# Kernel tuning notes

Measured on AMD Instinct MI355X. Metric: run time of the kernel, lower is better.

Reference implementation:

```python
import jax, jax.numpy as jnp
import numpy as np

N, K, CIN, HID, COUT, E, MH = 8192, 200, 512, 256, 40, 5, 64
KG = K // E
EPS = 1e-5


def setup_inputs() -> dict:
    key = jax.random.key(0)
    ks = jax.random.split(key, 20)
    inp = {
        "X": jax.random.normal(ks[0], (N, CIN), jnp.float32),
        "La": jax.random.uniform(ks[1], (K,), jnp.float32),
        "U": jax.random.normal(ks[2], (N, K), jnp.float32),
        # 5 EigenExperts, each mlp = Linear(1,64) -> ReLU -> Linear(64,64) -> ReLU -> Linear(64,1)
        "eW1": jax.random.normal(ks[3], (E, MH), jnp.float32) * 0.5,
        "eb1": jax.random.normal(ks[4], (E, MH), jnp.float32) * 0.1,
        "eW2": jax.random.normal(ks[5], (E, MH, MH), jnp.float32) * (1.0 / np.sqrt(MH)),
        "eb2": jax.random.normal(ks[6], (E, MH), jnp.float32) * 0.1,
        "eW3": jax.random.normal(ks[7], (E, MH), jnp.float32) * (1.0 / np.sqrt(MH)),
        "eb3": jax.random.normal(ks[8], (E,), jnp.float32) * 0.1,
        # gate: Linear(5,5) -> ReLU -> Linear(5,5) -> Softmax
        "gW1": jax.random.normal(ks[9], (E, E), jnp.float32) * 0.4,
        "gb1": jax.random.normal(ks[10], (E,), jnp.float32) * 0.1,
        "gW2": jax.random.normal(ks[11], (E, E), jnp.float32) * 0.4,
        "gb2": jax.random.normal(ks[12], (E,), jnp.float32) * 0.1,
        # W: Linear(in_channels, hidden_dim)
        "Ww": jax.random.normal(ks[13], (CIN, HID), jnp.float32) * (1.0 / np.sqrt(CIN)),
        "Wb": jax.random.normal(ks[14], (HID,), jnp.float32) * 0.1,
        # BatchNorm1d(hidden_dim), training-mode batch stats
        "bn_gamma": jnp.ones((HID,), jnp.float32),
        "bn_beta": jnp.zeros((HID,), jnp.float32),
        # MLP: Linear(hidden_dim, out_channels)
        "Mw": jax.random.normal(ks[15], (HID, COUT), jnp.float32) * (1.0 / np.sqrt(HID)),
        "Mb": jax.random.normal(ks[16], (COUT,), jnp.float32) * 0.1,
    }
    return inp


def reference(X, La, U, eW1, eb1, eW2, eb2, eW3, eb3, gW1, gb1, gW2, gb2, Ww, Wb, bn_gamma, bn_beta, Mw, Mb):
    n, k = U.shape
    e = eW1.shape[0]
    kg = k // e
    # group eigenvector columns: U[:, i*kg:(i+1)*kg] for expert i -> [n, e, kg]
    Ue = U.reshape(n, e, kg)
    # EigenExpert tiny MLP applied elementwise over entries of each column, then mean over nodes
    h1 = jax.nn.relu(jnp.einsum('nek,eh->nekh', Ue, eW1) + eb1[None, :, None, :])
    h2 = jax.nn.relu(jnp.einsum('nekh,ehg->nekg', h1, eW2) + eb2[None, :, None, :])
    v = jnp.einsum('nekh,eh->nek', h2, eW3) + eb3[None, :, None]
    V = v.mean(axis=0)                      # [e, kg] importance per eigenvector
    # gate on per-group mean eigenvalue
    stats = La.reshape(e, kg).mean(axis=1)  # [e]
    g = jax.nn.relu(stats @ gW1 + gb1) @ gW2 + gb2
    g = jax.nn.softmax(g, axis=-1)          # [e]
    # sum_i g_i * U_i diag(V_i) U_i^T == (U * s) @ U^T with per-column scale s
    s = (g[:, None] * V).reshape(k)         # [k]
    A = (U * s[None, :]) @ U.T              # [n, n]
    out = A @ X                             # [n, cin]
    hidden = out @ Ww + Wb                  # [n, hid]
    mu = hidden.mean(axis=0)
    var = hidden.var(axis=0)                # biased, as torch BN uses for normalization
    h = (hidden - mu) * jax.lax.rsqrt(var + EPS) * bn_gamma + bn_beta
    h = jax.nn.relu(h)                      # dropout is identity (eval)
    logits = h @ Mw + Mb
    return jax.nn.log_softmax(logits, axis=1), hidden
```

## Files before the change

### kernel.cpp

```cpp
#include <hip/hip_runtime.h>
#include <hip/hip_bf16.h>

#define N_    8192
#define K_    200
#define CIN_  512
#define HID_  256
#define COUT_ 40
#define E_    5
#define MH_   64
#define KG_   40
#define EPS_  1e-5f

#define WS_VSUM  0
#define WS_BNSUM 256
#define WS_T     768
#define WS_S     103168
#define WS_G     103424

typedef __bf16 bf16x8 __attribute__((ext_vector_type(8)));
typedef _Float16 f16x2 __attribute__((ext_vector_type(2)));
typedef _Float16 f16x8 __attribute__((ext_vector_type(8)));
typedef float  f32x16 __attribute__((ext_vector_type(16)));

__device__ __forceinline__ uint packbf(float a, float b) {
    union { __bf16 h[2]; uint u; } p;
    p.h[0] = (__bf16)a; p.h[1] = (__bf16)b;
    return p.u;
}

union UB { uint4 q; bf16x8 v; };
union UHF { f16x2 h2[4]; f16x8 v; };

__global__ __launch_bounds__(256) void k_expert(
    const float* __restrict__ U,
    const float* __restrict__ eW1, const float* __restrict__ eb1,
    const float* __restrict__ eW2, const float* __restrict__ eb2,
    const float* __restrict__ eW3, const float* __restrict__ eb3,
    float* __restrict__ Vsum)
{
    const int e   = blockIdx.x;
    const int tid = threadIdx.x;
    const int w   = tid >> 6;
    const int l   = tid & 63;
    const int lo  = l & 31;
    const int hi  = l >> 5;

    __shared__ f16x2 sW1h[32], sb1h[32];
    __shared__ float sb2s[MH_], sW3s[MH_];
    __shared__ float colsum[KG_];

    if (tid < 32) {
        f16x2 w2; w2.x = (_Float16)eW1[e*MH_ + 2*tid]; w2.y = (_Float16)eW1[e*MH_ + 2*tid + 1];
        sW1h[tid] = w2;
        f16x2 b2; b2.x = (_Float16)eb1[e*MH_ + 2*tid]; b2.y = (_Float16)eb1[e*MH_ + 2*tid + 1];
        sb1h[tid] = b2;
    }
    if (tid < MH_) {
        sb2s[tid] = eb2[e*MH_ + tid];
        sW3s[tid] = eW3[e*MH_ + tid];
    }
    if (tid < KG_) colsum[tid] = 0.f;
    const float b3 = eb3[e];

    UHF fa[2][4];
    {
        const float* W2e = eW2 + e*MH_*MH_;
        #pragma unroll
        for (int mt = 0; mt < 2; ++mt) {
            const int grow = mt*32 + lo;
            #pragma unroll
            for (int t = 0; t < 4; ++t) {
                const int k0 = 16*t + 8*hi;
                #pragma unroll
                for (int r = 0; r < 4; ++r) {
                    f16x2 p;
                    p.x = (_Float16)W2e[(k0+2*r  )*MH_ + grow];
                    p.y = (_Float16)W2e[(k0+2*r+1)*MH_ + grow];
                    fa[mt][t].h2[r] = p;
                }
            }
        }
    }
    __syncthreads();

    float uu[4]; int kgs[4];
    {
        const int idx0 = (blockIdx.y*16 + w)*64 + l;
        int n = idx0 / KG_, kg = idx0 - n*KG_;
        #pragma unroll
        for (int it = 0; it < 4; ++it) {
            uu[it]  = U[n*K_ + e*KG_ + kg];
            kgs[it] = kg;
            kg += 16; if (kg >= KG_) { kg -= KG_; n += 1; }
            n += 6;
        }
    }

    const f16x2 z2 = {(_Float16)0.f, (_Float16)0.f};

    #pragma unroll
    for (int it = 0; it < 4; ++it) {
        const float ucol0 = __shfl(uu[it], lo);
        const float ucol1 = __shfl(uu[it], 32 + lo);
        f16x2 u20; u20.x = (_Float16)ucol0; u20.y = (_Float16)ucol0;
        f16x2 u21; u21.x = (_Float16)ucol1; u21.y = (_Float16)ucol1;

        f32x16 acc00 = {0}; f32x16 acc10 = {0};
        f32x16 acc01 = {0}; f32x16 acc11 = {0};
        #pragma unroll
        for (int t = 0; t < 4; ++t) {
            const int kp = 8*t + 4*hi;
            UHF b0, b1;
            #pragma unroll
            for (int r = 0; r < 4; ++r) {
                const f16x2 w1  = sW1h[kp + r];
                const f16x2 b1c = sb1h[kp + r];
                b0.h2[r] = __builtin_elementwise_max(u20*w1 + b1c, z2);
                b1.h2[r] = __builtin_elementwise_max(u21*w1 + b1c, z2);
            }
            acc00 = __builtin_amdgcn_mfma_f32_32x32x16_f16(fa[0][t].v, b0.v, acc00, 0, 0, 0);
            acc10 = __builtin_amdgcn_mfma_f32_32x32x16_f16(fa[1][t].v, b0.v, acc10, 0, 0, 0);
            acc01 = __builtin_amdgcn_mfma_f32_32x32x16_f16(fa[0][t].v, b1.v, acc01, 0, 0, 0);
            acc11 = __builtin_amdgcn_mfma_f32_32x32x16_f16(fa[1][t].v, b1.v, acc11, 0, 0, 0);
        }

        float vs0 = 0.f, vs1 = 0.f;
        #pragma unroll
        for (int r = 0; r < 16; ++r) {
            const int gb  = (r & 3) + 8*(r >> 2) + 4*hi;
            const float b2a = sb2s[gb],      w3a = sW3s[gb];
            const float b2b = sb2s[32 + gb], w3b = sW3s[32 + gb];
            vs0 += fmaxf(acc00[r] + b2a, 0.f)*w3a + fmaxf(acc10[r] + b2b, 0.f)*w3b;
            vs1 += fmaxf(acc01[r] + b2a, 0.f)*w3a + fmaxf(acc11[r] + b2b, 0.f)*w3b;
        }
        vs0 += __shfl_xor(vs0, 32);
        vs1 += __shfl_xor(vs1, 32);

        const float myv = (hi ? vs1 : vs0) + b3;
        atomicAdd(&colsum[kgs[it]], myv);
    }

    __syncthreads();
    if (tid < KG_) atomicAdd(&Vsum[e*KG_ + tid], colsum[tid]);
}

__global__ void k_gate(
    const float* __restrict__ La,
    const float* __restrict__ gW1, const float* __restrict__ gb1,
    const float* __restrict__ gW2, const float* __restrict__ gb2,
    const float* __restrict__ Vsum, float* __restrict__ s)
{
    __shared__ float sg[E_];
    const int tid = threadIdx.x;
    if (tid == 0) {
        float stats[E_], g1[E_], g2[E_];
        for (int e = 0; e < E_; ++e) {
            float acc = 0.f;
            for (int k = 0; k < KG_; ++k) acc += La[e*KG_ + k];
            stats[e] = acc * (1.0f/KG_);
        }
        for (int j = 0; j < E_; ++j) {
            float acc = gb1[j];
            for (int i = 0; i < E_; ++i) acc += stats[i]*gW1[i*E_ + j];
            g1[j] = fmaxf(acc, 0.f);
        }
        float m = -1e30f;
        for (int j = 0; j < E_; ++j) {
            float acc = gb2[j];
            for (int i = 0; i < E_; ++i) acc += g1[i]*gW2[i*E_ + j];
            g2[j] = acc;
            m = fmaxf(m, acc);
        }
        float ssum = 0.f;
        for (int j = 0; j < E_; ++j) { g2[j] = expf(g2[j]-m); ssum += g2[j]; }
        for (int j = 0; j < E_; ++j) sg[j] = g2[j] / ssum;
    }
    __syncthreads();
    if (tid < K_) s[tid] = sg[tid / KG_] * Vsum[tid] * (1.0f/N_);
}

__global__ __launch_bounds__(256) void k_utx(
    const float* __restrict__ U, const float* __restrict__ X,
    float* __restrict__ P)
{
    const int nc0 = blockIdx.x * 64;
    const int mc0 = blockIdx.y * 64;
    const int ks  = blockIdx.z;
    const int r0  = ks * 512;
    const int tid = threadIdx.x;
    const int w   = tid >> 6, l = tid & 63, lo = l & 31, hi = l >> 5;
    const int mq  = w >> 1, nq = w & 1;

    __shared__ uint sU[2][32][68];
    __shared__ uint sX[2][32][68];

    const int rpA = tid >> 4;
    const int rpB = rpA + 16;
    const int c4  = tid & 15;
    const int mcA = mc0 + 4*c4;
    const int xcA = nc0 + 4*c4;
    const int UMAX = N_*K_ - 4;

    float4 uA0,uA1,uB0,uB1,xA0,xA1,xB0,xB1;

#define UTX_LD(chunk) {                                                       \
    const int rb_ = r0 + 64*(chunk);                                          \
    uA0 = *reinterpret_cast<const float4*>(&U[min((rb_+2*rpA  )*K_ + mcA, UMAX)]); \
    uA1 = *reinterpret_cast<const float4*>(&U[min((rb_+2*rpA+1)*K_ + mcA, UMAX)]); \
    uB0 = *reinterpret_cast<const float4*>(&U[min((rb_+2*rpB  )*K_ + mcA, UMAX)]); \
    uB1 = *reinterpret_cast<const float4*>(&U[min((rb_+2*rpB+1)*K_ + mcA, UMAX)]); \
    xA0 = *reinterpret_cast<const float4*>(&X[(rb_+2*rpA  )*CIN_ + xcA]);     \
    xA1 = *reinterpret_cast<const float4*>(&X[(rb_+2*rpA+1)*CIN_ + xcA]);     \
    xB0 = *reinterpret_cast<const float4*>(&X[(rb_+2*rpB  )*CIN_ + xcA]);     \
    xB1 = *reinterpret_cast<const float4*>(&X[(rb_+2*rpB+1)*CIN_ + xcA]); }

#define UTX_WR(buf) {                                                         \
    uint4 p_;                                                                 \
    p_.x = packbf(uA0.x,uA1.x); p_.y = packbf(uA0.y,uA1.y);                   \
    p_.z = packbf(uA0.z,uA1.z); p_.w = packbf(uA0.w,uA1.w);                   \
    *reinterpret_cast<uint4*>(&sU[buf][rpA][4*c4]) = p_;                      \
    p_.x = packbf(uB0.x,uB1.x); p_.y = packbf(uB0.y,uB1.y);                   \
    p_.z = packbf(uB0.z,uB1.z); p_.w = packbf(uB0.w,uB1.w);                   \
    *reinterpret_cast<uint4*>(&sU[buf][rpB][4*c4]) = p_;                      \
    p_.x = packbf(xA0.x,xA1.x); p_.y = packbf(xA0.y,xA1.y);                   \
    p_.z = packbf(xA0.z,xA1.z); p_.w = packbf(xA0.w,xA1.w);                   \
    *reinterpret_cast<uint4*>(&sX[buf][rpA][4*c4]) = p_;                      \
    p_.x = packbf(xB0.x,xB1.x); p_.y = packbf(xB0.y,xB1.y);                   \
    p_.z = packbf(xB0.z,xB1.z); p_.w = packbf(xB0.w,xB1.w);                   \
    *reinterpret_cast<uint4*>(&sX[buf][rpB][4*c4]) = p_; }

#define UTX_MM(buf) {                                                         \
    _Pragma("unroll") for (int ksi = 0; ksi < 4; ++ksi) {                     \
        const int rp0_ = 8*ksi + 4*hi;                                        \
        UB a_, b_;                                                            \
        a_.q.x = sU[buf][rp0_+0][32*mq+lo];                                   \
        a_.q.y = sU[buf][rp0_+1][32*mq+lo];                                   \
        a_.q.z = sU[buf][rp0_+2][32*mq+lo];                                   \
        a_.q.w = sU[buf][rp0_+3][32*mq+lo];                                   \
        b_.q.x = sX[buf][rp0_+0][32*nq+lo];                                   \
        b_.q.y = sX[buf][rp0_+1][32*nq+lo];                                   \
        b_.q.z = sX[buf][rp0_+2][32*nq+lo];                                   \
        b_.q.w = sX[buf][rp0_+3][32*nq+lo];                                   \
        acc = __builtin_amdgcn_mfma_f32_32x32x16_bf16(a_.v, b_.v, acc, 0,0,0); } }

    f32x16 acc = {0};
    UTX_LD(0);
    UTX_WR(0);
    __syncthreads();
    #pragma unroll
    for (int t = 0; t < 8; ++t) {
        if (t < 7) UTX_LD(t+1);
        UTX_MM(t & 1);
        if (t < 7) UTX_WR((t+1) & 1);
        __syncthreads();
    }

    #pragma unroll
    for (int r = 0; r < 16; ++r) {
        const int mrow = mc0 + mq*32 + (r & 3) + 8*(r >> 2) + 4*hi;
        const int ncol = nc0 + nq*32 + lo;
        P[(ks*256 + mrow)*512 + ncol] = acc[r];
    }
#undef UTX_LD
#undef UTX_WR
#undef UTX_MM
}

__global__ __launch_bounds__(256) void k_red(
    const float* __restrict__ P, float* __restrict__ T)
{
    const int j  = blockIdx.x*256 + threadIdx.x;
    const int m  = j >> 7;
    const int c4 = j & 127;
    float4 s4 = {0.f, 0.f, 0.f, 0.f};
    for (int ks = 0; ks < 16; ++ks) {
        const float4 v = *reinterpret_cast<const float4*>(&P[(ks*256 + m)*512 + 4*c4]);
        s4.x += v.x; s4.y += v.y; s4.z += v.z; s4.w += v.w;
    }
    *reinterpret_cast<float4*>(&T[m*512 + 4*c4]) = s4;
}

__global__ __launch_bounds__(256) void k_g(
    const float* __restrict__ T, const float* __restrict__ Ww,
    float* __restrict__ G)
{
    const int k0  = blockIdx.x * 4;
    const int c   = threadIdx.x;
    __shared__ float4 sT4[4][128];

    for (int j = threadIdx.x; j < 512; j += 256) {
        const int r = j >> 7, c4 = j & 127;
        sT4[r][c4] = reinterpret_cast<const float4*>(T)[(k0+r)*128 + c4];
    }
    __syncthreads();

    float a0 = 0.f, a1 = 0.f, a2 = 0.f, a3 = 0.f;
    for (int ci4 = 0; ci4 < 128; ++ci4) {
        const float w0 = Ww[(4*ci4+0)*HID_ + c];
        const float w1 = Ww[(4*ci4+1)*HID_ + c];
        const float w2 = Ww[(4*ci4+2)*HID_ + c];
        const float w3 = Ww[(4*ci4+3)*HID_ + c];
        float4 t;
        t = sT4[0][ci4]; a0 += t.x*w0 + t.y*w1 + t.z*w2 + t.w*w3;
        t = sT4[1][ci4]; a1 += t.x*w0 + t.y*w1 + t.z*w2 + t.w*w3;
        t = sT4[2][ci4]; a2 += t.x*w0 + t.y*w1 + t.z*w2 + t.w*w3;
        t = sT4[3][ci4]; a3 += t.x*w0 + t.y*w1 + t.z*w2 + t.w*w3;
    }
    G[(k0+0)*HID_ + c] = a0;
    G[(k0+1)*HID_ + c] = a1;
    G[(k0+2)*HID_ + c] = a2;
    G[(k0+3)*HID_ + c] = a3;
}

__global__ __launch_bounds__(256) void k_hidden(
    const float* __restrict__ U, const float* __restrict__ s,
    const float* __restrict__ G, const float* __restrict__ Wb,
    float* __restrict__ hid, float* __restrict__ bnsum)
{
    const int c0  = blockIdx.x * 32;
    const int n0  = blockIdx.y * 128;
    const int tid = threadIdx.x;
    const int w   = tid >> 6;
    const int l   = tid & 63;
    const int lo  = l & 31;
    const int hi  = l >> 5;

    __shared__ uint  sA[104][129];
    __shared__ uint  sB[104][33];
    __shared__ float ss[208];

    if (tid < 208) ss[tid] = (tid < K_) ? s[tid] : 0.f;
    __syncthreads();

    #pragma unroll
    for (int u = 0; u < 13; ++u) {
        const int j  = tid + u*256;
        const int m  = j & 127, kq = j >> 7;
        float4 a = {0,0,0,0}, b = {0,0,0,0};
        if (kq < 25) {
            a = *reinterpret_cast<const float4*>(&U[(n0+m)*K_ + 8*kq]);
            b = *reinterpret_cast<const float4*>(&U[(n0+m)*K_ + 8*kq + 4]);
            a.x *= ss[8*kq+0]; a.y *= ss[8*kq+1]; a.z *= ss[8*kq+2]; a.w *= ss[8*kq+3];
            b.x *= ss[8*kq+4]; b.y *= ss[8*kq+5]; b.z *= ss[8*kq+6]; b.w *= ss[8*kq+7];
        }
        sA[4*kq+0][m] = packbf(a.x, a.y);
        sA[4*kq+1][m] = packbf(a.z, a.w);
        sA[4*kq+2][m] = packbf(b.x, b.y);
        sA[4*kq+3][m] = packbf(b.z, b.w);
    }
    for (int j = tid; j < 832; j += 256) {
        const int c = j & 31, kq = j >> 5;
        float g[8];
        #pragma unroll
        for (int i = 0; i < 8; ++i)
            g[i] = (kq < 25) ? G[(8*kq+i)*HID_ + c0 + c] : 0.f;
        sB[4*kq+0][c] = packbf(g[0], g[1]);
        sB[4*kq+1][c] = packbf(g[2], g[3]);
        sB[4*kq+2][c] = packbf(g[4], g[5]);
        sB[4*kq+3][c] = packbf(g[6], g[7]);
    }
    __syncthreads();

    f32x16 acc = {0};
    #pragma unroll
    for (int t = 0; t < 13; ++t) {
        const int rp0 = 8*t + 4*hi;
        UB a_, b_;
        a_.q.x = sA[rp0+0][32*w + lo];
        a_.q.y = sA[rp0+1][32*w + lo];
        a_.q.z = sA[rp0+2][32*w + lo];
        a_.q.w = sA[rp0+3][32*w + lo];
        b_.q.x = sB[rp0+0][lo];
        b_.q.y = sB[rp0+1][lo];
        b_.q.z = sB[rp0+2][lo];
        b_.q.w = sB[rp0+3][lo];
        acc = __builtin_amdgcn_mfma_f32_32x32x16_bf16(a_.v, b_.v, acc, 0, 0, 0);
    }

    const float wb = Wb[c0 + lo];
    float sm = 0.f, sq = 0.f;
    #pragma unroll
    for (int r = 0; r < 16; ++r) {
        const int row = 32*w + (r & 3) + 8*(r >> 2) + 4*hi;
        const float h = acc[r] + wb;
        hid[(n0+row)*HID_ + c0 + lo] = h;
        sm += h; sq += h*h;
    }
    sm += __shfl_xor(sm, 32); sq += __shfl_xor(sq, 32);
    if (hi == 0) {
        atomicAdd(&bnsum[c0 + lo],        sm);
        atomicAdd(&bnsum[HID_ + c0 + lo], sq);
    }
}

__global__ __launch_bounds__(256) void k_logits(
    const float* __restrict__ hid, const float* __restrict__ bnsum,
    const float* __restrict__ gamma, const float* __restrict__ beta,
    const float* __restrict__ Mw, const float* __restrict__ Mb,
    float* __restrict__ outls)
{
    __shared__ float sc[HID_], sh[HID_], sMb[COUT_];
    __shared__ float sMw[HID_][COUT_];
    __shared__ float sPart[8][32][41];

    const int tid = threadIdx.x;
    const int r   = tid & 31;
    const int sl  = tid >> 5;

    {
        const float sm = bnsum[tid], sq = bnsum[HID_+tid];
        const float mu  = sm * (1.0f/N_);
        const float var = sq * (1.0f/N_) - mu*mu;
        const float a   = gamma[tid] * rsqrtf(var + EPS_);
        sc[tid] = a;
        sh[tid] = beta[tid] - mu*a;
    }
    for (int j = tid; j < HID_*COUT_/4; j += 256)
        reinterpret_cast<float4*>(&sMw[0][0])[j] = reinterpret_cast<const float4*>(Mw)[j];
    if (tid < COUT_) sMb[tid] = Mb[tid];
    __syncthreads();

    const int n  = blockIdx.x*32 + r;
    const int cb = sl * 32;
    float acc[COUT_];
    #pragma unroll
    for (int j = 0; j < COUT_; ++j) acc[j] = 0.f;

    const float4* hrow = reinterpret_cast<const float4*>(&hid[n*HID_ + cb]);
    #pragma unroll
    for (int c4 = 0; c4 < 8; ++c4) {
        const float4 h4 = hrow[c4];
        const float hv[4] = {h4.x, h4.y, h4.z, h4.w};
        #pragma unroll
        for (int q = 0; q < 4; ++q) {
            const int c = cb + 4*c4 + q;
            const float hn = fmaxf(hv[q]*sc[c] + sh[c], 0.f);
            #pragma unroll
            for (int j0 = 0; j0 < COUT_; j0 += 4) {
                const float4 wv = *reinterpret_cast<const float4*>(&sMw[c][j0]);
                acc[j0+0] += hn*wv.x; acc[j0+1] += hn*wv.y;
                acc[j0+2] += hn*wv.z; acc[j0+3] += hn*wv.w;
            }
        }
    }
    #pragma unroll
    for (int j = 0; j < COUT_; ++j) sPart[sl][r][j] = acc[j];
    __syncthreads();

    if (tid < 32) {
        const int n2 = blockIdx.x*32 + tid;
        float a2[COUT_];
        #pragma unroll
        for (int j = 0; j < COUT_; ++j) {
            float sum = sMb[j];
            #pragma unroll
            for (int s2 = 0; s2 < 8; ++s2) sum += sPart[s2][tid][j];
            a2[j] = sum;
        }
        float m = -1e30f;
        #pragma unroll
        for (int j = 0; j < COUT_; ++j) m = fmaxf(m, a2[j]);
        float ssum = 0.f;
        #pragma unroll
        for (int j = 0; j < COUT_; ++j) ssum += expf(a2[j] - m);
        const float lse = m + logf(ssum);
        #pragma unroll
        for (int j = 0; j < COUT_; ++j)
            outls[n2*COUT_ + j] = a2[j] - lse;
    }
}

extern "C" void kernel_launch(void* const* d_in, const int* in_sizes, int n_in,
                              void* d_out, int out_size, void* d_ws, size_t ws_size,
                              hipStream_t stream)
{
    const float* X        = (const float*)d_in[0];
    const float* La       = (const float*)d_in[1];
    const float* U        = (const float*)d_in[2];
    const float* eW1      = (const float*)d_in[3];
    const float* eb1      = (const float*)d_in[4];
    const float* eW2      = (const float*)d_in[5];
    const float* eb2      = (const float*)d_in[6];
    const float* eW3      = (const float*)d_in[7];
    const float* eb3      = (const float*)d_in[8];
    const float* gW1      = (const float*)d_in[9];
    const float* gb1      = (const float*)d_in[10];
    const float* gW2      = (const float*)d_in[11];
    const float* gb2      = (const float*)d_in[12];
    const float* Ww       = (const float*)d_in[13];
    const float* Wb       = (const float*)d_in[14];
    const float* bn_gamma = (const float*)d_in[15];
    const float* bn_beta  = (const float*)d_in[16];
    const float* Mw       = (const float*)d_in[17];
    const float* Mb       = (const float*)d_in[18];

    float* out   = (float*)d_out;
    float* ws    = (float*)d_ws;
    float* Vsum  = ws + WS_VSUM;
    float* bnsum = ws + WS_BNSUM;
    float* T     = ws + WS_T;
    float* s     = ws + WS_S;
    float* G     = ws + WS_G;

    float* outls = out;
    float* hid   = out + N_*COUT_;
    float* P     = out;

    (void)hipMemsetAsync(ws, 0, (size_t)768 * sizeof(float), stream);

    k_utx   <<<dim3(8, 4, 16), 256, 0, stream>>>(U, X, P);
    k_expert<<<dim3(E_, 320),  256, 0, stream>>>(U, eW1, eb1, eW2, eb2, eW3, eb3, Vsum);
    k_gate  <<<1,   256, 0, stream>>>(La, gW1, gb1, gW2, gb2, Vsum, s);
    k_red   <<<100, 256, 0, stream>>>(P, T);
    k_g     <<<50,  256, 0, stream>>>(T, Ww, G);
    k_hidden<<<dim3(8, 64), 256, 0, stream>>>(U, s, G, Wb, hid, bnsum);
    k_logits<<<256, 256, 0, stream>>>(hid, bnsum, bn_gamma, bn_beta, Mw, Mb, outls);
}
```

Measured before the change: 228.1 us.

## Restructure expert MLP kernel: one column per MFMA tile, bias-seeded accumulators

```diff
diff --git a/kernel.cpp b/kernel.cpp
--- a/kernel.cpp
+++ b/kernel.cpp
@@ -47,7 +47,7 @@
 
     __shared__ f16x2 sW1h[32], sb1h[32];
     __shared__ float sb2s[MH_], sW3s[MH_];
-    __shared__ float colsum[KG_];
+    __shared__ float colsum[4][48];
 
     if (tid < 32) {
         f16x2 w2; w2.x = (_Float16)eW1[e*MH_ + 2*tid]; w2.y = (_Float16)eW1[e*MH_ + 2*tid + 1];
@@ -59,7 +59,7 @@
         sb2s[tid] = eb2[e*MH_ + tid];
         sW3s[tid] = eW3[e*MH_ + tid];
     }
-    if (tid < KG_) colsum[tid] = 0.f;
+    if (tid < 192) colsum[tid / 48][tid % 48] = 0.f;
     const float b3 = eb3[e];
 
     UHF fa[2][4];
@@ -83,65 +83,67 @@
     }
     __syncthreads();
 
+    f32x16 ci0, ci1;
+    #pragma unroll
+    for (int r = 0; r < 16; ++r) {
+        const int gb = (r & 3) + 8*(r >> 2) + 4*hi;
+        ci0[r] = sb2s[gb];
+        ci1[r] = sb2s[32 + gb];
+    }
+
     float uu[4]; int kgs[4];
-    {
-        const int idx0 = (blockIdx.y*16 + w)*64 + l;
-        int n = idx0 / KG_, kg = idx0 - n*KG_;
-        #pragma unroll
-        for (int it = 0; it < 4; ++it) {
-            uu[it]  = U[n*K_ + e*KG_ + kg];
-            kgs[it] = kg;
-            kg += 16; if (kg >= KG_) { kg -= KG_; n += 1; }
-            n += 6;
-        }
+    const int tile0 = blockIdx.y*16 + w*4;
+    #pragma unroll
+    for (int it = 0; it < 4; ++it) {
+        const int idx = (tile0 + it)*32 + lo;
+        const int n   = idx / KG_;
+        const int kg  = idx - n*KG_;
+        uu[it]  = U[n*K_ + e*KG_ + kg];
+        kgs[it] = kg;
     }
 
     const f16x2 z2 = {(_Float16)0.f, (_Float16)0.f};
 
     #pragma unroll
     for (int it = 0; it < 4; ++it) {
-        const float ucol0 = __shfl(uu[it], lo);
-        const float ucol1 = __shfl(uu[it], 32 + lo);
-        f16x2 u20; u20.x = (_Float16)ucol0; u20.y = (_Float16)ucol0;
-        f16x2 u21; u21.x = (_Float16)ucol1; u21.y = (_Float16)ucol1;
-
-        f32x16 acc00 = {0}; f32x16 acc10 = {0};
-        f32x16 acc01 = {0}; f32x16 acc11 = {0};
+        f16x2 u2; u2.x = (_Float16)uu[it]; u2.y = u2.x;
+
+        f32x16 a0, a1;
         #pragma unroll
         for (int t = 0; t < 4; ++t) {
             const int kp = 8*t + 4*hi;
-            UHF b0, b1;
+            UHF b;
             #pragma unroll
-            for (int r = 0; r < 4; ++r) {
-                const f16x2 w1  = sW1h[kp + r];
-                const f16x2 b1c = sb1h[kp + r];
-                b0.h2[r] = __builtin_elementwise_max(u20*w1 + b1c, z2);
-                b1.h2[r] = __builtin_elementwise_max(u21*w1 + b1c, z2);
+            for (int r = 0; r < 4; ++r)
+                b.h2[r] = __builtin_elementwise_max(u2*sW1h[kp + r] + sb1h[kp + r], z2);
+            if (t == 0) {
+                a0 = __builtin_amdgcn_mfma_f32_32x32x16_f16(fa[0][0].v, b.v, ci0, 0, 0, 0);
+                a1 = __builtin_amdgcn_mfma_f32_32x32x16_f16(fa[1][0].v, b.v, ci1, 0, 0, 0);
+            } else {
+                a0 = __builtin_amdgcn_mfma_f32_32x32x16_f16(fa[0][t].v, b.v, a0, 0, 0, 0);
+                a1 = __builtin_amdgcn_mfma_f32_32x32x16_f16(fa[1][t].v, b.v, a1, 0, 0, 0);
             }
-            acc00 = __builtin_amdgcn_mfma_f32_32x32x16_f16(fa[0][t].v, b0.v, acc00, 0, 0, 0);
-            acc10 = __builtin_amdgcn_mfma_f32_32x32x16_f16(fa[1][t].v, b0.v, acc10, 0, 0, 0);
-            acc01 = __builtin_amdgcn_mfma_f32_32x32x16_f16(fa[0][t].v, b1.v, acc01, 0, 0, 0);
-            acc11 = __builtin_amdgcn_mfma_f32_32x32x16_f16(fa[1][t].v, b1.v, acc11, 0, 0, 0);
-        }
-
-        float vs0 = 0.f, vs1 = 0.f;
-        #pragma unroll
-        for (int r = 0; r < 16; ++r) {
-            const int gb  = (r & 3) + 8*(r >> 2) + 4*hi;
-            const float b2a = sb2s[gb],      w3a = sW3s[gb];
-            const float b2b = sb2s[32 + gb], w3b = sW3s[32 + gb];
-            vs0 += fmaxf(acc00[r] + b2a, 0.f)*w3a + fmaxf(acc10[r] + b2b, 0.f)*w3b;
-            vs1 += fmaxf(acc01[r] + b2a, 0.f)*w3a + fmaxf(acc11[r] + b2b, 0.f)*w3b;
-        }
-        vs0 += __shfl_xor(vs0, 32);
-        vs1 += __shfl_xor(vs1, 32);
-
-        const float myv = (hi ? vs1 : vs0) + b3;
-        atomicAdd(&colsum[kgs[it]], myv);
-    }
-
-    __syncthreads();
-    if (tid < KG_) atomicAdd(&Vsum[e*KG_ + tid], colsum[tid]);
+        }
+
+        float p0 = 0.f, p1 = 0.f, p2 = 0.f, p3 = 0.f;
+        #pragma unroll
+        for (int r = 0; r < 16; r += 2) {
+            const int g0 = (r & 3) + 8*(r >> 2) + 4*hi;
+            const int g1 = ((r+1) & 3) + 8*((r+1) >> 2) + 4*hi;
+            p0 += fmaxf(a0[r],   0.f) * sW3s[g0];
+            p1 += fmaxf(a1[r],   0.f) * sW3s[32 + g0];
+            p2 += fmaxf(a0[r+1], 0.f) * sW3s[g1];
+            p3 += fmaxf(a1[r+1], 0.f) * sW3s[32 + g1];
+        }
+        float vs = (p0 + p1) + (p2 + p3);
+        vs += __shfl_xor(vs, 32);
+        if (hi == 0) atomicAdd(&colsum[w][kgs[it]], vs + b3);
+    }
+
+    __syncthreads();
+    if (tid < KG_)
+        atomicAdd(&Vsum[e*KG_ + tid],
+                  colsum[0][tid] + colsum[1][tid] + colsum[2][tid] + colsum[3][tid]);
 }
 
 __global__ void k_gate(
@@ -509,7 +511,7 @@
     (void)hipMemsetAsync(ws, 0, (size_t)768 * sizeof(float), stream);
 
     k_utx   <<<dim3(8, 4, 16), 256, 0, stream>>>(U, X, P);
-    k_expert<<<dim3(E_, 320),  256, 0, stream>>>(U, eW1, eb1, eW2, eb2, eW3, eb3, Vsum);
+    k_expert<<<dim3(E_, 640),  256, 0, stream>>>(U, eW1, eb1, eW2, eb2, eW3, eb3, Vsum);
     k_gate  <<<1,   256, 0, stream>>>(La, gW1, gb1, gW2, gb2, Vsum, s);
     k_red   <<<100, 256, 0, stream>>>(P, T);
     k_g     <<<50,  256, 0, stream>>>(T, Ww, G);
```

Result: faster. 210.7 us (-7.7%).
